# Optimization experiments

Hardware: AMD Instinct MI355X
Metric: run time of the kernel (lower is better)

Reference implementation:

```python
import jax, jax.numpy as jnp
import numpy as np

DEPTH, DIM, DFF, VOCAB = 4, 512, 2048, 4096
EPS = 1e-5

def layernorm(x, w, b):
    mu = jnp.mean(x, axis=-1, keepdims=True)
    var = jnp.mean((x - mu) ** 2, axis=-1, keepdims=True)
    return (x - mu) * jax.lax.rsqrt(var + EPS) * w + b

def sconv(x, phazor_c, last_conv_c):
    # x: [B,L,dim] real; phazor_c, last_conv_c: [dim] complex
    B, L, D = x.shape
    r = jnp.abs(phazor_c)
    p = jnp.tanh(r) * jnp.exp(1j * jnp.angle(phazor_c))          # [dim]
    prog = p[None, :] ** jnp.arange(L, dtype=jnp.float32)[:, None]  # [L,dim]
    filt_fft = jnp.fft.fft(prog, n=2 * L, axis=0)                # [2L,dim]
    x_fft = jnp.fft.fft(x.astype(jnp.complex64), n=2 * L, axis=1)  # [B,2L,dim]
    conv = jnp.fft.ifft(filt_fft[None] * x_fft, axis=1)[:, :L]   # [B,L,dim]
    conv = conv + last_conv_c[None, None, :] * prog[None] * p[None, None, :]
    return conv.real.astype(x.dtype)

def setup_inputs() -> dict:
    key = jax.random.key(0)
    ks = jax.random.split(key, 20)
    f32 = jnp.float32
    inp = {}
    inp['x'] = jax.random.normal(ks[0], (2, 4096, VOCAB), dtype=f32)
    inp['Win'] = jax.random.normal(ks[1], (DIM, VOCAB), dtype=f32) * VOCAB ** -0.5
    inp['bin'] = jnp.zeros((DIM,), f32)
    inp['ln1_w'] = jnp.ones((DEPTH, DIM), f32)
    inp['ln1_b'] = jnp.zeros((DEPTH, DIM), f32)
    # phazor init: exp(2*pi*i*arange/dim)*|randn|
    ang = 2 * np.pi * jnp.arange(DIM, dtype=f32) / DIM
    mag = jnp.abs(jax.random.normal(ks[2], (DEPTH, DIM), dtype=f32))
    inp['phz_re'] = mag * jnp.cos(ang)[None]
    inp['phz_im'] = mag * jnp.sin(ang)[None]
    inp['lc_re'] = jax.random.normal(ks[3], (DEPTH, DIM), dtype=f32)
    inp['lc_im'] = jax.random.normal(ks[4], (DEPTH, DIM), dtype=f32)
    inp['sc_lin'] = jnp.ones((DEPTH, DIM), f32)
    inp['ln2_w'] = jnp.ones((DEPTH, DIM), f32)
    inp['ln2_b'] = jnp.zeros((DEPTH, DIM), f32)
    inp['W1'] = jax.random.normal(ks[5], (DEPTH, DFF, DIM), dtype=f32) * DIM ** -0.5
    inp['b1'] = jnp.zeros((DEPTH, DFF), f32)
    inp['W2'] = jax.random.normal(ks[6], (DEPTH, DIM, DFF), dtype=f32) * DFF ** -0.5
    inp['b2'] = jnp.zeros((DEPTH, DIM), f32)
    inp['lnl_w'] = jnp.ones((DIM,), f32)
    inp['lnl_b'] = jnp.zeros((DIM,), f32)
    inp['Wout'] = jax.random.normal(ks[7], (VOCAB, DIM), dtype=f32) * DIM ** -0.5
    inp['bout'] = jnp.zeros((VOCAB,), f32)
    return inp

def _forward(x, Win, bin, ln1_w, ln1_b, phz_re, phz_im, lc_re, lc_im, sc_lin,
             ln2_w, ln2_b, W1, b1, W2, b2, lnl_w, lnl_b, Wout, bout):
    h = jnp.einsum('blv,dv->bld', x, Win) + bin  # token_in

    def body(h, p):
        l1w, l1b, pr, pi, lr, li, scl, l2w, l2b, w1, b1_, w2, b2_ = p
        y = jax.nn.silu(layernorm(h, l1w, l1b))
        y = sconv(y, pr + 1j * pi, lr + 1j * li)
        h = h + y * scl
        y = layernorm(h, l2w, l2b)
        y = jax.nn.silu(jnp.einsum('bld,fd->blf', y, w1) + b1_)
        y = jnp.einsum('blf,df->bld', y, w2) + b2_
        return h + y, None

    xs = (ln1_w, ln1_b, phz_re, phz_im, lc_re, lc_im, sc_lin,
          ln2_w, ln2_b, W1, b1, W2, b2)
    h, _ = jax.lax.scan(body, h, xs)
    h = layernorm(h, lnl_w, lnl_b)
    return jnp.einsum('bld,vd->blv', h, Wout) + bout

def reference(x, Win, bin, ln1_w, ln1_b, phz_re, phz_im, lc_re, lc_im, sc_lin,
              ln2_w, ln2_b, W1, b1, W2, b2, lnl_w, lnl_b, Wout, bout):
    return _forward(x, Win, bin, ln1_w, ln1_b, phz_re, phz_im, lc_re, lc_im,
                    sc_lin, ln2_w, ln2_b, W1, b1, W2, b2, lnl_w, lnl_b, Wout, bout)
```

## Files before the change

kernel.cpp:

```cpp
#include <hip/hip_runtime.h>
#include <hip/hip_bf16.h>
#include <cstdint>
#include <cstddef>

#define DEPTH 4
#define DIM 512
#define DFF 2048
#define VOCAB 4096
#define NB 2
#define LSEQ 4096
#define MR (NB*LSEQ)
#define EPSL 1e-5f
#define NC 128
#define TCH 32

typedef __attribute__((ext_vector_type(8))) short  s8v;
typedef __attribute__((ext_vector_type(4))) float  f4v;
typedef __attribute__((ext_vector_type(8))) __bf16 bf8v;

__device__ __forceinline__ unsigned short f2b(float f) {
  union { float f; unsigned int u; } v; v.f = f;
  unsigned int r = v.u + 0x7FFFu + ((v.u >> 16) & 1u);
  return (unsigned short)(r >> 16);
}

__device__ __forceinline__ void gld16(const void* g, void* l) {
  __builtin_amdgcn_global_load_lds(
      (const __attribute__((address_space(1))) unsigned int*)(uintptr_t)g,
      (__attribute__((address_space(3))) unsigned int*)(uintptr_t)l,
      16, 0, 0);
}

__global__ void __launch_bounds__(256) cvt_f32_bf16(
    const float* __restrict__ in, unsigned short* __restrict__ out, int n8)
{
  int i = blockIdx.x * 256 + threadIdx.x;
  if (i >= n8) return;
  const f4v* p = (const f4v*)(in + (size_t)i * 8);
  f4v a = p[0], b = p[1];
  s8v o;
  o[0]=(short)f2b(a[0]); o[1]=(short)f2b(a[1]); o[2]=(short)f2b(a[2]); o[3]=(short)f2b(a[3]);
  o[4]=(short)f2b(b[0]); o[5]=(short)f2b(b[1]); o[6]=(short)f2b(b[2]); o[7]=(short)f2b(b[3]);
  *(s8v*)(out + (size_t)i * 8) = o;
}

template<int MODE>
__global__ void __launch_bounds__(256) ln_kernel(
    const float* __restrict__ x, const float* __restrict__ w, const float* __restrict__ b,
    float* __restrict__ outf, unsigned short* __restrict__ outb)
{
  int row  = blockIdx.x * 4 + (threadIdx.x >> 6);
  int lane = threadIdx.x & 63;
  const float* xp = x + (size_t)row * DIM + lane * 8;
  f4v v0 = *(const f4v*)xp;
  f4v v1 = *(const f4v*)(xp + 4);
  float s = 0.f, s2 = 0.f;
#pragma unroll
  for (int j = 0; j < 4; ++j) { s += v0[j]; s2 += v0[j]*v0[j]; s += v1[j]; s2 += v1[j]*v1[j]; }
#pragma unroll
  for (int off = 32; off; off >>= 1) { s += __shfl_xor(s, off, 64); s2 += __shfl_xor(s2, off, 64); }
  float mu = s * (1.f / DIM);
  float rs = rsqrtf(s2 * (1.f / DIM) - mu * mu + EPSL);
  int c = lane * 8;
  float ov[8];
#pragma unroll
  for (int j = 0; j < 8; ++j) {
    float xv = (j < 4) ? v0[j] : v1[j - 4];
    float o = (xv - mu) * rs * w[c + j] + b[c + j];
    if (MODE == 0) o = o / (1.f + __expf(-o));
    ov[j] = o;
  }
  if (MODE == 0) {
    f4v o0 = {ov[0], ov[1], ov[2], ov[3]};
    f4v o1 = {ov[4], ov[5], ov[6], ov[7]};
    *(f4v*)(outf + (size_t)row * DIM + c)     = o0;
    *(f4v*)(outf + (size_t)row * DIM + c + 4) = o1;
  } else {
    s8v o;
#pragma unroll
    for (int j = 0; j < 8; ++j) o[j] = (short)f2b(ov[j]);
    *(s8v*)(outb + (size_t)row * DIM + c) = o;
  }
}

__device__ __forceinline__ void phz2p(float re, float im, float& pre, float& pim) {
  float r = sqrtf(re * re + im * im);
  float t = (r > 1e-20f) ? (tanhf(r) / r) : 1.0f;
  pre = t * re; pim = t * im;
}

__global__ void __launch_bounds__(256) scan_a(
    const float* __restrict__ y, const float* __restrict__ pr, const float* __restrict__ pi,
    float* __restrict__ stA)
{
  int d = blockIdx.z * 256 + threadIdx.x;
  int b = blockIdx.y, c = blockIdx.x;
  float pre, pim; phz2p(pr[d], pi[d], pre, pim);
  const float* yp = y + ((size_t)b * LSEQ + (size_t)c * TCH) * DIM + d;
  float sre = 0.f, sim = 0.f;
#pragma unroll 8
  for (int j = 0; j < TCH; ++j) {
    float xv = yp[(size_t)j * DIM];
    float nre = fmaf(pre, sre, fmaf(-pim, sim, xv));
    float nim = fmaf(pre, sim, pim * sre);
    sre = nre; sim = nim;
  }
  size_t o = (((size_t)b * NC + c) * DIM + d) * 2;
  stA[o] = sre; stA[o + 1] = sim;
}

__global__ void __launch_bounds__(256) scan_b(
    const float* __restrict__ stA, float* __restrict__ carry,
    const float* __restrict__ pr, const float* __restrict__ pi,
    const float* __restrict__ lcr, const float* __restrict__ lci)
{
  int idx = blockIdx.x * 256 + threadIdx.x;
  int b = idx >> 9, d = idx & (DIM - 1);
  float pre, pim; phz2p(pr[d], pi[d], pre, pim);
  float qre = pre, qim = pim;
#pragma unroll
  for (int t = 0; t < 5; ++t) { float nr = qre*qre - qim*qim; float ni = 2.f*qre*qim; qre = nr; qim = ni; }
  float cre = lcr[d], cim = lci[d];
#pragma unroll 4
  for (int c = 0; c < NC; ++c) {
    size_t o = (((size_t)b * NC + c) * DIM + d) * 2;
    carry[o] = cre; carry[o + 1] = cim;
    float are = stA[o], aim = stA[o + 1];
    float nr = fmaf(qre, cre, fmaf(-qim, cim, are));
    float ni = fmaf(qre, cim, fmaf(qim, cre, aim));
    cre = nr; cim = ni;
  }
}

__global__ void __launch_bounds__(256) scan_c(
    const float* __restrict__ y, float* __restrict__ h, const float* __restrict__ carry,
    const float* __restrict__ pr, const float* __restrict__ pi,
    const float* __restrict__ scl)
{
  int d = blockIdx.z * 256 + threadIdx.x;
  int b = blockIdx.y, c = blockIdx.x;
  float pre, pim; phz2p(pr[d], pi[d], pre, pim);
  size_t o = (((size_t)b * NC + c) * DIM + d) * 2;
  float sre = carry[o], sim = carry[o + 1];
  float sc = scl[d];
  const float* yp = y + ((size_t)b * LSEQ + (size_t)c * TCH) * DIM + d;
  float*       hp = h + ((size_t)b * LSEQ + (size_t)c * TCH) * DIM + d;
#pragma unroll 8
  for (int j = 0; j < TCH; ++j) {
    float xv = yp[(size_t)j * DIM];
    float nre = fmaf(pre, sre, fmaf(-pim, sim, xv));
    float nim = fmaf(pre, sim, pim * sre);
    sre = nre; sim = nim;
    hp[(size_t)j * DIM] += sre * sc;
  }
}

template<int EPI>
__global__ void __launch_bounds__(256, 2) gemm_bt(
    const unsigned short* __restrict__ A, const unsigned short* __restrict__ Bm,
    const float* __restrict__ bias,
    float* __restrict__ Cf, unsigned short* __restrict__ Cb,
    int N, int K)
{
  __shared__ unsigned short As[2][128 * 32];
  __shared__ unsigned short Bs[2][128 * 32];
  const int tid  = threadIdx.x;
  const int lane = tid & 63, wave = tid >> 6;
  const int wm = wave >> 1, wn = wave & 1;
  const int fr = lane & 15, fq = lane >> 4;
  const int m0 = blockIdx.y * 128, n0 = blockIdx.x * 128;

  f4v acc[4][4];
#pragma unroll
  for (int i = 0; i < 4; ++i)
#pragma unroll
    for (int j = 0; j < 4; ++j) acc[i][j] = (f4v){0.f, 0.f, 0.f, 0.f};

  const int nkt = K >> 5;

  auto stage = [&](int buf, int k0) {
    const unsigned short* Ab = A  + (size_t)m0 * K + k0;
    const unsigned short* Bb = Bm + (size_t)n0 * K + k0;
#pragma unroll
    for (int r = 0; r < 2; ++r) {
      int idx = r * 256 + tid;
      int row = idx >> 2, col = (idx & 3) << 3;
      gld16(Ab + (size_t)row * K + col, &As[buf][idx * 8]);
      gld16(Bb + (size_t)row * K + col, &Bs[buf][idx * 8]);
    }
  };

  stage(0, 0);
  __syncthreads();

  for (int kt = 0; kt < nkt; ++kt) {
    int cur = kt & 1;
    if (kt + 1 < nkt) stage(cur ^ 1, (kt + 1) << 5);
    bf8v av[4], bv[4];
#pragma unroll
    for (int i = 0; i < 4; ++i) {
      av[i] = *(const bf8v*)&As[cur][(wm * 64 + i * 16 + fr) * 32 + fq * 8];
      bv[i] = *(const bf8v*)&Bs[cur][(wn * 64 + i * 16 + fr) * 32 + fq * 8];
    }
#pragma unroll
    for (int i = 0; i < 4; ++i)
#pragma unroll
      for (int j = 0; j < 4; ++j)
        acc[i][j] = __builtin_amdgcn_mfma_f32_16x16x32_bf16(av[i], bv[j], acc[i][j], 0, 0, 0);
    __syncthreads();
  }

#pragma unroll
  for (int j = 0; j < 4; ++j) {
    const int col = n0 + wn * 64 + j * 16 + fr;
    const float bsv = bias[col];
#pragma unroll
    for (int i = 0; i < 4; ++i) {
#pragma unroll
      for (int r = 0; r < 4; ++r) {
        const int row = m0 + wm * 64 + i * 16 + fq * 4 + r;
        const size_t off = (size_t)row * N + col;
        float v = acc[i][j][r] + bsv;
        if constexpr (EPI == 0) {
          Cf[off] = v;
        } else if constexpr (EPI == 1) {
          float sv = v / (1.f + __expf(-v));
          Cb[off] = f2b(sv);
        } else {
          Cf[off] = Cf[off] + v;
        }
      }
    }
  }
}

extern "C" void kernel_launch(void* const* d_in, const int* in_sizes, int n_in,
                              void* d_out, int out_size, void* d_ws, size_t ws_size,
                              hipStream_t stream)
{
  (void)in_sizes; (void)n_in; (void)out_size; (void)ws_size;
  const float* x    = (const float*)d_in[0];
  const float* Win  = (const float*)d_in[1];
  const float* bin  = (const float*)d_in[2];
  const float* ln1w = (const float*)d_in[3];
  const float* ln1b = (const float*)d_in[4];
  const float* phzr = (const float*)d_in[5];
  const float* phzi = (const float*)d_in[6];
  const float* lcr  = (const float*)d_in[7];
  const float* lci  = (const float*)d_in[8];
  const float* scl  = (const float*)d_in[9];
  const float* ln2w = (const float*)d_in[10];
  const float* ln2b = (const float*)d_in[11];
  const float* W1   = (const float*)d_in[12];
  const float* b1   = (const float*)d_in[13];
  const float* W2   = (const float*)d_in[14];
  const float* b2   = (const float*)d_in[15];
  const float* lnlw = (const float*)d_in[16];
  const float* lnlb = (const float*)d_in[17];
  const float* Wout = (const float*)d_in[18];
  const float* bout = (const float*)d_in[19];

  char* wsp = (char*)d_ws;
  auto alloc = [&](size_t bytes) { char* p = wsp; wsp += (bytes + 255) & ~(size_t)255; return p; };
  float*          h     = (float*)alloc((size_t)MR * DIM * 4);
  float*          y     = (float*)alloc((size_t)MR * DIM * 4);
  unsigned short* yb    = (unsigned short*)alloc((size_t)MR * DIM * 2);
  unsigned short* Winb  = (unsigned short*)alloc((size_t)DIM * VOCAB * 2);
  unsigned short* W1b   = (unsigned short*)alloc((size_t)DEPTH * DFF * DIM * 2);
  unsigned short* W2b   = (unsigned short*)alloc((size_t)DEPTH * DIM * DFF * 2);
  unsigned short* Woutb = (unsigned short*)alloc((size_t)VOCAB * DIM * 2);
  float*          stA   = (float*)alloc((size_t)NB * NC * DIM * 2 * 4);
  float*          carry = (float*)alloc((size_t)NB * NC * DIM * 2 * 4);

  unsigned short* xb   = (unsigned short*)d_out;
  unsigned short* act1 = (unsigned short*)d_out;

  dim3 blk(256);
  cvt_f32_bf16<<<dim3(((size_t)MR * VOCAB) / 2048), blk, 0, stream>>>(x, xb, (int)(((size_t)MR * VOCAB) / 8));
  cvt_f32_bf16<<<dim3((DIM * VOCAB) / 2048), blk, 0, stream>>>(Win, Winb, DIM * VOCAB / 8);
  cvt_f32_bf16<<<dim3((DEPTH * DFF * DIM) / 2048), blk, 0, stream>>>(W1, W1b, DEPTH * DFF * DIM / 8);
  cvt_f32_bf16<<<dim3((DEPTH * DFF * DIM) / 2048), blk, 0, stream>>>(W2, W2b, DEPTH * DIM * DFF / 8);
  cvt_f32_bf16<<<dim3((VOCAB * DIM) / 2048), blk, 0, stream>>>(Wout, Woutb, VOCAB * DIM / 8);

  gemm_bt<0><<<dim3(DIM / 128, MR / 128), blk, 0, stream>>>(xb, Winb, bin, h, nullptr, DIM, VOCAB);

  for (int l = 0; l < DEPTH; ++l) {
    ln_kernel<0><<<dim3(MR / 4), blk, 0, stream>>>(h, ln1w + l * DIM, ln1b + l * DIM, y, nullptr);
    scan_a<<<dim3(NC, NB, DIM / 256), blk, 0, stream>>>(y, phzr + l * DIM, phzi + l * DIM, stA);
    scan_b<<<dim3((NB * DIM) / 256), blk, 0, stream>>>(stA, carry, phzr + l * DIM, phzi + l * DIM,
                                                       lcr + l * DIM, lci + l * DIM);
    scan_c<<<dim3(NC, NB, DIM / 256), blk, 0, stream>>>(y, h, carry, phzr + l * DIM, phzi + l * DIM,
                                                        scl + l * DIM);
    ln_kernel<1><<<dim3(MR / 4), blk, 0, stream>>>(h, ln2w + l * DIM, ln2b + l * DIM, nullptr, yb);
    gemm_bt<1><<<dim3(DFF / 128, MR / 128), blk, 0, stream>>>(yb, W1b + (size_t)l * DFF * DIM,
                                                              b1 + l * DFF, nullptr, act1, DFF, DIM);
    gemm_bt<2><<<dim3(DIM / 128, MR / 128), blk, 0, stream>>>(act1, W2b + (size_t)l * DIM * DFF,
                                                              b2 + l * DIM, h, nullptr, DIM, DFF);
  }
  ln_kernel<1><<<dim3(MR / 4), blk, 0, stream>>>(h, lnlw, lnlb, nullptr, yb);
  gemm_bt<0><<<dim3(VOCAB / 128, MR / 128), blk, 0, stream>>>(yb, Woutb, bout, (float*)d_out, nullptr,
                                                              VOCAB, DIM);
}
```

Baseline: 672.6 us.

## Fuse input fp32-to-bf16 conversion into GEMM, add BN=64 tiles and block swizzle

The separate conversion of the large 2x4096x4096 fp32 input to bf16 is removed. The token-in GEMM now loads fp32 A tiles into registers and converts them while storing to shared memory, which avoids a full write and read of the bf16 copy. The GEMM is templated on N tile width, so the narrow-N GEMMs (N=512) use 64-wide tiles to launch more blocks, and a block-index remap spreads neighbouring workgroups. LayerNorm weight and bias loads are vectorised; the launch-bounds occupancy hints change and register pressure may rise.

```diff
diff --git a/kernel.cpp b/kernel.cpp
--- a/kernel.cpp
+++ b/kernel.cpp
@@ -62,11 +62,15 @@
   float mu = s * (1.f / DIM);
   float rs = rsqrtf(s2 * (1.f / DIM) - mu * mu + EPSL);
   int c = lane * 8;
+  f4v w0 = *(const f4v*)(w + c), w1 = *(const f4v*)(w + c + 4);
+  f4v b0 = *(const f4v*)(b + c), b1 = *(const f4v*)(b + c + 4);
   float ov[8];
 #pragma unroll
   for (int j = 0; j < 8; ++j) {
     float xv = (j < 4) ? v0[j] : v1[j - 4];
-    float o = (xv - mu) * rs * w[c + j] + b[c + j];
+    float wv = (j < 4) ? w0[j] : w1[j - 4];
+    float bv = (j < 4) ? b0[j] : b1[j - 4];
+    float o = (xv - mu) * rs * wv + bv;
     if (MODE == 0) o = o / (1.f + __expf(-o));
     ov[j] = o;
   }
@@ -155,64 +159,116 @@
   }
 }
 
-template<int EPI>
-__global__ void __launch_bounds__(256, 2) gemm_bt(
-    const unsigned short* __restrict__ A, const unsigned short* __restrict__ Bm,
+template<int EPI, int BN, int AF32>
+__global__ void __launch_bounds__(256, BN == 64 ? 2 : 3) gemm_bt(
+    const void* __restrict__ Ap, const unsigned short* __restrict__ Bm,
     const float* __restrict__ bias,
     float* __restrict__ Cf, unsigned short* __restrict__ Cb,
     int N, int K)
 {
+  constexpr int WN = BN / 2;
+  constexpr int NJ = WN / 16;
   __shared__ unsigned short As[2][128 * 32];
-  __shared__ unsigned short Bs[2][128 * 32];
+  __shared__ unsigned short Bs[2][BN * 32];
   const int tid  = threadIdx.x;
   const int lane = tid & 63, wave = tid >> 6;
   const int wm = wave >> 1, wn = wave & 1;
   const int fr = lane & 15, fq = lane >> 4;
-  const int m0 = blockIdx.y * 128, n0 = blockIdx.x * 128;
-
-  f4v acc[4][4];
+
+  int bx, by;
+  {
+    int gx = gridDim.x;
+    int nwg = gx * gridDim.y;
+    int b = blockIdx.y * gx + blockIdx.x;
+    int lid = (b & 7) * (nwg >> 3) + (b >> 3);
+    bx = lid % gx; by = lid / gx;
+  }
+  const int m0 = by * 128, n0 = bx * BN;
+
+  f4v acc[4][NJ];
 #pragma unroll
   for (int i = 0; i < 4; ++i)
 #pragma unroll
-    for (int j = 0; j < 4; ++j) acc[i][j] = (f4v){0.f, 0.f, 0.f, 0.f};
+    for (int j = 0; j < NJ; ++j) acc[i][j] = (f4v){0.f, 0.f, 0.f, 0.f};
 
   const int nkt = K >> 5;
 
-  auto stage = [&](int buf, int k0) {
-    const unsigned short* Ab = A  + (size_t)m0 * K + k0;
-    const unsigned short* Bb = Bm + (size_t)n0 * K + k0;
+  f4v areg[2][2];
+  auto loadA = [&](int k0) {
+    const float* Ab = (const float*)Ap + (size_t)m0 * K + k0;
+#pragma unroll
+    for (int r = 0; r < 2; ++r) {
+      int idx = r * 256 + tid;
+      int row = idx >> 2, col = (idx & 3) << 3;
+      const float* p = Ab + (size_t)row * K + col;
+      areg[r][0] = *(const f4v*)p;
+      areg[r][1] = *(const f4v*)(p + 4);
+    }
+  };
+  auto writeA = [&](int buf) {
+#pragma unroll
+    for (int r = 0; r < 2; ++r) {
+      int idx = r * 256 + tid;
+      s8v o;
+#pragma unroll
+      for (int j = 0; j < 4; ++j) {
+        o[j]     = (short)f2b(areg[r][0][j]);
+        o[4 + j] = (short)f2b(areg[r][1][j]);
+      }
+      *(s8v*)&As[buf][idx * 8] = o;
+    }
+  };
+  auto stageA16 = [&](int buf, int k0) {
+    const unsigned short* Ab = (const unsigned short*)Ap + (size_t)m0 * K + k0;
 #pragma unroll
     for (int r = 0; r < 2; ++r) {
       int idx = r * 256 + tid;
       int row = idx >> 2, col = (idx & 3) << 3;
       gld16(Ab + (size_t)row * K + col, &As[buf][idx * 8]);
+    }
+  };
+  auto stageB = [&](int buf, int k0) {
+    const unsigned short* Bb = Bm + (size_t)n0 * K + k0;
+#pragma unroll
+    for (int r = 0; r < BN / 64; ++r) {
+      int idx = r * 256 + tid;
+      int row = idx >> 2, col = (idx & 3) << 3;
       gld16(Bb + (size_t)row * K + col, &Bs[buf][idx * 8]);
     }
   };
 
-  stage(0, 0);
+  if constexpr (AF32) loadA(0); else stageA16(0, 0);
+  stageB(0, 0);
+  if constexpr (AF32) writeA(0);
   __syncthreads();
 
   for (int kt = 0; kt < nkt; ++kt) {
     int cur = kt & 1;
-    if (kt + 1 < nkt) stage(cur ^ 1, (kt + 1) << 5);
-    bf8v av[4], bv[4];
-#pragma unroll
-    for (int i = 0; i < 4; ++i) {
+    bool pf = (kt + 1 < nkt);
+    if (pf) {
+      if constexpr (AF32) loadA((kt + 1) << 5);
+      else stageA16(cur ^ 1, (kt + 1) << 5);
+      stageB(cur ^ 1, (kt + 1) << 5);
+    }
+    bf8v av[4], bv[NJ];
+#pragma unroll
+    for (int i = 0; i < 4; ++i)
       av[i] = *(const bf8v*)&As[cur][(wm * 64 + i * 16 + fr) * 32 + fq * 8];
-      bv[i] = *(const bf8v*)&Bs[cur][(wn * 64 + i * 16 + fr) * 32 + fq * 8];
-    }
+#pragma unroll
+    for (int j = 0; j < NJ; ++j)
+      bv[j] = *(const bf8v*)&Bs[cur][(wn * WN + j * 16 + fr) * 32 + fq * 8];
 #pragma unroll
     for (int i = 0; i < 4; ++i)
 #pragma unroll
-      for (int j = 0; j < 4; ++j)
+      for (int j = 0; j < NJ; ++j)
         acc[i][j] = __builtin_amdgcn_mfma_f32_16x16x32_bf16(av[i], bv[j], acc[i][j], 0, 0, 0);
+    if (pf) { if constexpr (AF32) writeA(cur ^ 1); }
     __syncthreads();
   }
 
 #pragma unroll
-  for (int j = 0; j < 4; ++j) {
-    const int col = n0 + wn * 64 + j * 16 + fr;
+  for (int j = 0; j < NJ; ++j) {
+    const int col = n0 + wn * WN + j * 16 + fr;
     const float bsv = bias[col];
 #pragma unroll
     for (int i = 0; i < 4; ++i) {
@@ -272,17 +328,16 @@
   float*          stA   = (float*)alloc((size_t)NB * NC * DIM * 2 * 4);
   float*          carry = (float*)alloc((size_t)NB * NC * DIM * 2 * 4);
 
-  unsigned short* xb   = (unsigned short*)d_out;
   unsigned short* act1 = (unsigned short*)d_out;
 
   dim3 blk(256);
-  cvt_f32_bf16<<<dim3(((size_t)MR * VOCAB) / 2048), blk, 0, stream>>>(x, xb, (int)(((size_t)MR * VOCAB) / 8));
   cvt_f32_bf16<<<dim3((DIM * VOCAB) / 2048), blk, 0, stream>>>(Win, Winb, DIM * VOCAB / 8);
   cvt_f32_bf16<<<dim3((DEPTH * DFF * DIM) / 2048), blk, 0, stream>>>(W1, W1b, DEPTH * DFF * DIM / 8);
   cvt_f32_bf16<<<dim3((DEPTH * DFF * DIM) / 2048), blk, 0, stream>>>(W2, W2b, DEPTH * DIM * DFF / 8);
   cvt_f32_bf16<<<dim3((VOCAB * DIM) / 2048), blk, 0, stream>>>(Wout, Woutb, VOCAB * DIM / 8);
 
-  gemm_bt<0><<<dim3(DIM / 128, MR / 128), blk, 0, stream>>>(xb, Winb, bin, h, nullptr, DIM, VOCAB);
+  gemm_bt<0, 64, 1><<<dim3(DIM / 64, MR / 128), blk, 0, stream>>>(
+      x, Winb, bin, h, nullptr, DIM, VOCAB);
 
   for (int l = 0; l < DEPTH; ++l) {
     ln_kernel<0><<<dim3(MR / 4), blk, 0, stream>>>(h, ln1w + l * DIM, ln1b + l * DIM, y, nullptr);
@@ -292,12 +347,12 @@
     scan_c<<<dim3(NC, NB, DIM / 256), blk, 0, stream>>>(y, h, carry, phzr + l * DIM, phzi + l * DIM,
                                                         scl + l * DIM);
     ln_kernel<1><<<dim3(MR / 4), blk, 0, stream>>>(h, ln2w + l * DIM, ln2b + l * DIM, nullptr, yb);
-    gemm_bt<1><<<dim3(DFF / 128, MR / 128), blk, 0, stream>>>(yb, W1b + (size_t)l * DFF * DIM,
-                                                              b1 + l * DFF, nullptr, act1, DFF, DIM);
-    gemm_bt<2><<<dim3(DIM / 128, MR / 128), blk, 0, stream>>>(act1, W2b + (size_t)l * DIM * DFF,
-                                                              b2 + l * DIM, h, nullptr, DIM, DFF);
+    gemm_bt<1, 128, 0><<<dim3(DFF / 128, MR / 128), blk, 0, stream>>>(
+        yb, W1b + (size_t)l * DFF * DIM, b1 + l * DFF, nullptr, act1, DFF, DIM);
+    gemm_bt<2, 64, 0><<<dim3(DIM / 64, MR / 128), blk, 0, stream>>>(
+        act1, W2b + (size_t)l * DIM * DFF, b2 + l * DIM, h, nullptr, DIM, DFF);
   }
   ln_kernel<1><<<dim3(MR / 4), blk, 0, stream>>>(h, lnlw, lnlb, nullptr, yb);
-  gemm_bt<0><<<dim3(VOCAB / 128, MR / 128), blk, 0, stream>>>(yb, Woutb, bout, (float*)d_out, nullptr,
-                                                              VOCAB, DIM);
-}
+  gemm_bt<0, 128, 0><<<dim3(VOCAB / 128, MR / 128), blk, 0, stream>>>(
+      yb, Woutb, bout, (float*)d_out, nullptr, VOCAB, DIM);
+}
```

Result: faster. 649.9 us (-3.4%).
